# Kernel optimization log

Hardware: AMD Instinct MI355X
Metric: run time of the kernel (lower is better)

The kernel has to match this reference:

```python
import jax, jax.numpy as jnp
import numpy as np

TOP_K = 2
LB_WEIGHT = 0.01


def _ln(x, g, b, eps=1e-5):
    m = x.mean(-1, keepdims=True)
    v = ((x - m) ** 2).mean(-1, keepdims=True)
    return (x - m) * jax.lax.rsqrt(v + eps) * g + b


def setup_inputs() -> dict:
    key = jax.random.key(0)
    ks = iter(jax.random.split(key, 40))
    B, L, D, CT, CB, E, H = 8, 1024, 1024, 768, 64, 8, 1024
    ID = 3 * D           # concat(id, content_proj, collab_proj)
    GH = max(ID // 2, 128)  # 1536, router gate hidden

    def rn(shape, s=0.02):
        return jax.random.normal(next(ks), shape, jnp.float32) * s

    return {
        "id_emb": rn((B, L, D), 1.0),
        "content_emb": rn((B, L, CT), 1.0),
        "collab_emb": rn((B, L, CB), 1.0),
        "ln_ct_g": jnp.ones(CT), "ln_ct_b": jnp.zeros(CT),
        "ln_cb_g": jnp.ones(CB), "ln_cb_b": jnp.zeros(CB),
        "Wc": rn((CT, D)), "bc": jnp.zeros(D),
        "Wcb": rn((CB, D)), "bcb": jnp.zeros(D),
        "Wg1": rn((ID, GH)), "bg1": jnp.zeros(GH),
        "lng_g": jnp.ones(GH), "lng_b": jnp.zeros(GH),
        "Wg2": rn((GH, GH // 2)), "bg2": jnp.zeros(GH // 2),
        "Wg3": rn((GH // 2, E)), "bg3": jnp.zeros(E),
        "We1": rn((E, ID, H)), "be1": jnp.zeros((E, H)),
        "lne1_g": jnp.ones((E, H)), "lne1_b": jnp.zeros((E, H)),
        "We2": rn((E, H, H // 2)), "be2": jnp.zeros((E, H // 2)),
        "We3": rn((E, H // 2, H // 4)), "be3": jnp.zeros((E, H // 4)),
        "lne3_g": jnp.ones((E, H // 4)), "lne3_b": jnp.zeros((E, H // 4)),
        "Wout": rn((H // 4, D)), "bout": jnp.zeros(D),
        "alpha": jnp.full((1,), 0.1, jnp.float32),
    }


def reference(id_emb, content_emb, collab_emb, ln_ct_g, ln_ct_b, ln_cb_g, ln_cb_b,
              Wc, bc, Wcb, bcb, Wg1, bg1, lng_g, lng_b, Wg2, bg2, Wg3, bg3,
              We1, be1, lne1_g, lne1_b, We2, be2, We3, be3, lne3_g, lne3_b,
              Wout, bout, alpha):
    # --- input normalization + projection to d_model (eval mode: no noise/dropout) ---
    ct = _ln(content_emb, ln_ct_g, ln_ct_b) @ Wc + bc        # (B,L,D)
    cb = _ln(collab_emb, ln_cb_g, ln_cb_b) @ Wcb + bcb       # (B,L,D)
    x = jnp.concatenate([id_emb, ct, cb], axis=-1)           # (B,L,3D)

    # --- router: gate MLP -> softmax -> top-k -> renormalize ---
    g = jax.nn.relu(_ln(x @ Wg1 + bg1, lng_g, lng_b))
    g = jax.nn.relu(g @ Wg2 + bg2)
    probs = jax.nn.softmax(g @ Wg3 + bg3, axis=-1)           # (B,L,E)
    topv, topi = jax.lax.top_k(probs, TOP_K)                 # (B,L,K)
    w = topv / (topv.sum(-1, keepdims=True) + 1e-8)

    # --- experts (dense over E, then gather selected) ---
    h = jax.nn.relu(_ln(jnp.einsum('bld,edh->bleh', x, We1) + be1, lne1_g, lne1_b))
    h = jax.nn.relu(jnp.einsum('bleh,ehm->blem', h, We2) + be2)
    eo = _ln(jnp.einsum('blem,emo->bleo', h, We3) + be3, lne3_g, lne3_b)  # (B,L,E,H/4)
    sel = jnp.take_along_axis(eo, topi[..., None], axis=2)   # (B,L,K,H/4)
    comb = (sel * w[..., None]).sum(axis=2)                  # (B,L,H/4)

    # --- output projection + learnable-alpha residual ---
    fused = id_emb + alpha * (comb @ Wout + bout)            # (B,L,D)

    # --- load balancing loss (importance + entropy terms) ---
    E = probs.shape[-1]
    num_tokens = probs.shape[0] * probs.shape[1]
    counts = jnp.sum(jax.nn.one_hot(topi, E, dtype=jnp.float32), axis=(0, 1, 2))
    f = counts / num_tokens
    P = probs.mean(axis=(0, 1))
    importance = E * (f * P).sum()
    ent = -(P * jnp.log(P + 1e-8)).sum()
    max_ent = jnp.log(jnp.asarray(E, jnp.float32))
    lb_loss = (importance + (max_ent - ent) / max_ent) * LB_WEIGHT
    return fused, lb_loss
```

## Files before the change

### kernel.cpp

```cpp
#include <hip/hip_runtime.h>
#include <hip/hip_bf16.h>

using u16 = unsigned short;
typedef float f32x4 __attribute__((ext_vector_type(4)));
typedef short short8 __attribute__((ext_vector_type(8)));
typedef unsigned short ushort8 __attribute__((ext_vector_type(8)));

typedef __attribute__((address_space(1))) const unsigned int gu32;
typedef __attribute__((address_space(3))) unsigned int lu32;

__device__ __forceinline__ float b2f(u16 u) {
  unsigned v = ((unsigned)u) << 16;
  float f;
  __builtin_memcpy(&f, &v, 4);
  return f;
}
__device__ __forceinline__ u16 f2b(float f) {
  unsigned u;
  __builtin_memcpy(&u, &f, 4);
  unsigned r = (u + 0x7fffu + ((u >> 16) & 1u)) >> 16;
  return (u16)r;
}
__device__ __forceinline__ float ldv(float x) { return x; }
__device__ __forceinline__ float ldv(u16 x) { return b2f(x); }

__device__ __forceinline__ void gl_lds16(const void* g, void* l) {
  __builtin_amdgcn_global_load_lds((gu32*)g, (lu32*)l, 16, 0, 0);
}

template <int D, bool RELU, bool PEREXP, typename TIN>
__global__ void ln_rows(const TIN* __restrict__ in, u16* __restrict__ out,
                        const float* __restrict__ gamma, const float* __restrict__ beta,
                        const int* __restrict__ pairExp, const int* __restrict__ total) {
  constexpr int T = (D >= 256) ? 256 : 64;
  constexpr int VPT = D / T;
  int row = blockIdx.x;
  if constexpr (PEREXP) {
    if (row >= *total) return;
  }
  int t = threadIdx.x;
  const TIN* r = in + (size_t)row * D;
  float vals[VPT];
  float s = 0.f, ss = 0.f;
#pragma unroll
  for (int i = 0; i < VPT; ++i) {
    float v = ldv(r[t + i * T]);
    vals[i] = v;
    s += v;
    ss += v * v;
  }
#pragma unroll
  for (int m = 1; m < 64; m <<= 1) {
    s += __shfl_xor(s, m);
    ss += __shfl_xor(ss, m);
  }
  if constexpr (T == 256) {
    __shared__ float red[8];
    int wave = t >> 6, lane = t & 63;
    if (lane == 0) { red[wave] = s; red[4 + wave] = ss; }
    __syncthreads();
    s = red[0] + red[1] + red[2] + red[3];
    ss = red[4] + red[5] + red[6] + red[7];
  }
  float mean = s / (float)D;
  float var = ss / (float)D - mean * mean;
  var = fmaxf(var, 0.f);
  float rstd = 1.f / sqrtf(var + 1e-5f);
  const float* g = gamma;
  const float* b = beta;
  if constexpr (PEREXP) {
    int e = pairExp[row];
    g += (size_t)e * D;
    b += (size_t)e * D;
  }
  u16* o = out + (size_t)row * D;
#pragma unroll
  for (int i = 0; i < VPT; ++i) {
    int idx = t + i * T;
    float v = (vals[i] - mean) * rstd * g[idx] + b[idx];
    if constexpr (RELU) v = fmaxf(v, 0.f);
    o[idx] = f2b(v);
  }
}

__global__ void prepackT(const float* __restrict__ in, u16* __restrict__ out,
                         int K, int M) {
  __shared__ u16 tile[64 * 65];
  size_t zo = (size_t)blockIdx.z * K * M;
  const float* ip = in + zo;
  u16* op = out + zo;
  int m0 = blockIdx.x * 64, k0 = blockIdx.y * 64;
  int t = threadIdx.x;
#pragma unroll
  for (int h = 0; h < 4; ++h) {
    int u = t + h * 256;
    int kr = u >> 4, mc = (u & 15) * 4;
    f32x4 v = *(const f32x4*)(ip + (size_t)(k0 + kr) * M + m0 + mc);
#pragma unroll
    for (int i = 0; i < 4; ++i) tile[kr * 65 + mc + i] = f2b(v[i]);
  }
  __syncthreads();
#pragma unroll
  for (int h = 0; h < 2; ++h) {
    int u = t + h * 256;
    int mr = u >> 3, kc = (u & 7) * 8;
    ushort8 v;
#pragma unroll
    for (int i = 0; i < 8; ++i) v[i] = tile[(kc + i) * 65 + mr];
    *(ushort8*)(op + (size_t)(m0 + mr) * K + k0 + kc) = v;
  }
}

__global__ void copy_id3(const float* __restrict__ id, u16* __restrict__ xb3) {
  size_t i = ((size_t)blockIdx.x * 256 + threadIdx.x) * 8;
  size_t t = i >> 10, d = i & 1023;
  f32x4 a = *(const f32x4*)(id + i);
  f32x4 b = *(const f32x4*)(id + i + 4);
  ushort8 v;
#pragma unroll
  for (int j = 0; j < 4; ++j) { v[j] = f2b(a[j]); v[j + 4] = f2b(b[j]); }
  *(ushort8*)(xb3 + t * 3072 + d) = v;
}

#define BM 128
#define BN 128
#define BKK 64

template <int EPI, bool EXPERT, bool GATHER>
__global__ __launch_bounds__(256, 3)
void gemm_bf(const u16* __restrict__ A, const u16* __restrict__ Bt,
             const float* __restrict__ bias,
             u16* __restrict__ C, float* __restrict__ Cf,
             int K, int lda, int ldc,
             long strideB, int strideBias,
             const int* __restrict__ offA, const int* __restrict__ pairTok,
             const float* __restrict__ resid, const float* __restrict__ alphaPtr) {
  int gy = gridDim.y;
  int nwg = gridDim.x * gy;
  int id = blockIdx.x * gy + blockIdx.y;
  int q = nwg >> 3, r = nwg & 7;
  int xcd = id & 7, pos = id >> 3;
  int nid = (xcd < r) ? (xcd * (q + 1) + pos) : (r * (q + 1) + (xcd - r) * q + pos);
  int rowTile = (nid / gy) * BM;
  int colTile = (nid % gy) * BN;

  if constexpr (EXPERT) {
    if (rowTile >= offA[8]) return;
    int e = 0;
    while (rowTile >= offA[e + 1]) ++e;
    Bt += (size_t)e * strideB;
    bias += (size_t)e * strideBias;
  }

  __shared__ u16 As[BM * BKK];
  __shared__ u16 Bs[BN * BKK];

  int t = threadIdx.x;
  int lane = t & 63;
  int wv = t >> 6;
  int wr = wv >> 1, wc = wv & 1;
  int l15 = lane & 15, l4 = lane >> 4;

  int rowInLane = lane >> 3;
  int colLane = (lane & 7) * 8;
  const u16* aSrc[4];
  const u16* bSrc[4];
  u16* aDst[4];
  u16* bDst[4];
#pragma unroll
  for (int j = 0; j < 4; ++j) {
    int rr = j * 32 + wv * 8 + rowInLane;
    size_t aRow;
    if constexpr (GATHER) {
      aRow = (size_t)pairTok[rowTile + rr] * lda;
    } else {
      aRow = (size_t)(rowTile + rr) * lda;
    }
    aSrc[j] = A + aRow + colLane;
    bSrc[j] = Bt + (size_t)(colTile + rr) * K + colLane;
    aDst[j] = As + (j * 32 + wv * 8) * BKK;
    bDst[j] = Bs + (j * 32 + wv * 8) * BKK;
  }

  f32x4 zero4 = {0.f, 0.f, 0.f, 0.f};
  f32x4 acc[4][4];
#pragma unroll
  for (int m = 0; m < 4; ++m)
#pragma unroll
    for (int n = 0; n < 4; ++n) acc[m][n] = zero4;

  for (int k0 = 0; k0 < K; k0 += BKK) {
    __syncthreads();
#pragma unroll
    for (int j = 0; j < 4; ++j) gl_lds16(aSrc[j] + k0, aDst[j]);
#pragma unroll
    for (int j = 0; j < 4; ++j) gl_lds16(bSrc[j] + k0, bDst[j]);
    asm volatile("s_waitcnt vmcnt(0)" ::: "memory");
    __syncthreads();
    short8 af[4][2];
#pragma unroll
    for (int m = 0; m < 4; ++m)
#pragma unroll
      for (int ks = 0; ks < 2; ++ks)
        af[m][ks] = *(const short8*)&As[(wr * 64 + m * 16 + l15) * BKK + ks * 32 + l4 * 8];
#pragma unroll
    for (int n = 0; n < 4; ++n) {
      short8 bfr[2];
#pragma unroll
      for (int ks = 0; ks < 2; ++ks)
        bfr[ks] = *(const short8*)&Bs[(wc * 64 + n * 16 + l15) * BKK + ks * 32 + l4 * 8];
#pragma unroll
      for (int m = 0; m < 4; ++m)
#pragma unroll
        for (int ks = 0; ks < 2; ++ks)
          acc[m][n] = __builtin_amdgcn_mfma_f32_16x16x32_bf16(af[m][ks], bfr[ks], acc[m][n], 0, 0, 0);
    }
  }

  float alphaV = 0.f;
  if constexpr (EPI == 2) alphaV = alphaPtr[0];
#pragma unroll
  for (int n = 0; n < 4; ++n) {
    int col = colTile + wc * 64 + n * 16 + l15;
    float bv = bias[col];
#pragma unroll
    for (int m = 0; m < 4; ++m) {
      int r2 = rowTile + wr * 64 + m * 16 + l4 * 4;
#pragma unroll
      for (int j = 0; j < 4; ++j) {
        float v = acc[m][n][j] + bv;
        if constexpr (EPI == 1) v = fmaxf(v, 0.f);
        if constexpr (EPI == 2) {
          Cf[(size_t)(r2 + j) * ldc + col] =
              resid[(size_t)(r2 + j) * ldc + col] + alphaV * v;
        } else {
          C[(size_t)(r2 + j) * ldc + col] = f2b(v);
        }
      }
    }
  }
}

__global__ void router_kernel(const u16* __restrict__ g2, const float* __restrict__ Wg3,
                              const float* __restrict__ bg3, float* __restrict__ probs,
                              int* __restrict__ topi, float* __restrict__ wts) {
  int tok = blockIdx.x * 4 + (threadIdx.x >> 6);
  int lane = threadIdx.x & 63;
  const u16* row = g2 + (size_t)tok * 768;
  float acc[8];
#pragma unroll
  for (int e = 0; e < 8; ++e) acc[e] = 0.f;
  for (int j = lane; j < 768; j += 64) {
    float v = b2f(row[j]);
    f32x4 w0 = *(const f32x4*)(Wg3 + (size_t)j * 8);
    f32x4 w1 = *(const f32x4*)(Wg3 + (size_t)j * 8 + 4);
#pragma unroll
    for (int e = 0; e < 4; ++e) { acc[e] += v * w0[e]; acc[e + 4] += v * w1[e]; }
  }
#pragma unroll
  for (int e = 0; e < 8; ++e) {
#pragma unroll
    for (int m = 1; m < 64; m <<= 1) acc[e] += __shfl_xor(acc[e], m);
  }
  if (lane == 0) {
    float lg[8], mx = -3.4e38f;
#pragma unroll
    for (int e = 0; e < 8; ++e) {
      lg[e] = acc[e] + bg3[e];
      mx = fmaxf(mx, lg[e]);
    }
    float p[8], s = 0.f;
#pragma unroll
    for (int e = 0; e < 8; ++e) {
      p[e] = expf(lg[e] - mx);
      s += p[e];
    }
    float inv = 1.f / s;
#pragma unroll
    for (int e = 0; e < 8; ++e) {
      p[e] *= inv;
      probs[(size_t)tok * 8 + e] = p[e];
    }
    int i0 = 0;
    for (int e = 1; e < 8; ++e)
      if (p[e] > p[i0]) i0 = e;
    int i1 = (i0 == 0) ? 1 : 0;
    for (int e = 0; e < 8; ++e)
      if (e != i0 && p[e] > p[i1]) i1 = e;
    float w0 = p[i0], w1 = p[i1];
    float wsum = w0 + w1 + 1e-8f;
    topi[tok * 2] = i0;
    topi[tok * 2 + 1] = i1;
    wts[tok * 2] = w0 / wsum;
    wts[tok * 2 + 1] = w1 / wsum;
  }
}

__global__ void count_kernel(const int* __restrict__ topi, int* __restrict__ cnt,
                             int* __restrict__ offA, int* __restrict__ cursor) {
  __shared__ int c[8];
  int t = threadIdx.x;
  if (t < 8) c[t] = 0;
  __syncthreads();
  for (int i = t; i < 16384; i += 256) atomicAdd(&c[topi[i]], 1);
  __syncthreads();
  if (t == 0) {
    int off = 0;
    for (int e = 0; e < 8; ++e) {
      cnt[e] = c[e];
      offA[e] = off;
      cursor[e] = off;
      off += (c[e] + 127) & ~127;
    }
    offA[8] = off;
  }
}

__global__ void scatter_kernel(const int* __restrict__ topi, int* __restrict__ cursor,
                               int* __restrict__ pairTok, int* __restrict__ pairExp,
                               int* __restrict__ posOf) {
  int i = blockIdx.x * 256 + threadIdx.x;
  int e = topi[i];
  int pos = atomicAdd(&cursor[e], 1);
  pairTok[pos] = i >> 1;
  pairExp[pos] = e;
  posOf[i] = pos;
}

__global__ void padfill_kernel(const int* __restrict__ cnt, const int* __restrict__ offA,
                               int* __restrict__ pairTok, int* __restrict__ pairExp) {
  int e = blockIdx.x;
  int start = offA[e] + cnt[e];
  int end = offA[e + 1];
  for (int i = start + threadIdx.x; i < end; i += 256) {
    pairTok[i] = 0;
    pairExp[i] = e;
  }
}

__global__ void combine_kernel(const u16* __restrict__ eo, const int* __restrict__ posOf,
                               const float* __restrict__ wts, u16* __restrict__ comb) {
  int t = blockIdx.x, d = threadIdx.x;
  int p0 = posOf[t * 2], p1 = posOf[t * 2 + 1];
  float w0 = wts[t * 2], w1 = wts[t * 2 + 1];
  float v = w0 * b2f(eo[(size_t)p0 * 256 + d]) + w1 * b2f(eo[(size_t)p1 * 256 + d]);
  comb[(size_t)t * 256 + d] = f2b(v);
}

__global__ void lbloss_kernel(const float* __restrict__ probs, const int* __restrict__ cnt,
                              float* __restrict__ outp) {
  __shared__ float red[256];
  int t = threadIdx.x;
  float pl[8];
#pragma unroll
  for (int e = 0; e < 8; ++e) pl[e] = 0.f;
  for (int i = t; i < 8192; i += 256) {
#pragma unroll
    for (int e = 0; e < 8; ++e) pl[e] += probs[(size_t)i * 8 + e];
  }
  float P[8];
  for (int e = 0; e < 8; ++e) {
    red[t] = pl[e];
    __syncthreads();
    for (int s = 128; s > 0; s >>= 1) {
      if (t < s) red[t] += red[t + s];
      __syncthreads();
    }
    P[e] = red[0] / 8192.f;
    __syncthreads();
  }
  if (t == 0) {
    float imp = 0.f, ent = 0.f;
    for (int e = 0; e < 8; ++e) {
      float f = (float)cnt[e] / 8192.f;
      imp += f * P[e];
      ent -= P[e] * logf(P[e] + 1e-8f);
    }
    imp *= 8.f;
    float maxent = logf(8.f);
    outp[0] = (imp + (maxent - ent) / maxent) * 0.01f;
  }
}

extern "C" void kernel_launch(void* const* d_in, const int* in_sizes, int n_in,
                              void* d_out, int out_size, void* d_ws, size_t ws_size,
                              hipStream_t stream) {
  const float* id_emb   = (const float*)d_in[0];
  const float* content  = (const float*)d_in[1];
  const float* collab   = (const float*)d_in[2];
  const float* ln_ct_g  = (const float*)d_in[3];
  const float* ln_ct_b  = (const float*)d_in[4];
  const float* ln_cb_g  = (const float*)d_in[5];
  const float* ln_cb_b  = (const float*)d_in[6];
  const float* Wc       = (const float*)d_in[7];
  const float* bc       = (const float*)d_in[8];
  const float* Wcb      = (const float*)d_in[9];
  const float* bcb      = (const float*)d_in[10];
  const float* Wg1      = (const float*)d_in[11];
  const float* bg1      = (const float*)d_in[12];
  const float* lng_g    = (const float*)d_in[13];
  const float* lng_b    = (const float*)d_in[14];
  const float* Wg2      = (const float*)d_in[15];
  const float* bg2      = (const float*)d_in[16];
  const float* Wg3      = (const float*)d_in[17];
  const float* bg3      = (const float*)d_in[18];
  const float* We1      = (const float*)d_in[19];
  const float* be1      = (const float*)d_in[20];
  const float* lne1_g   = (const float*)d_in[21];
  const float* lne1_b   = (const float*)d_in[22];
  const float* We2      = (const float*)d_in[23];
  const float* be2      = (const float*)d_in[24];
  const float* We3      = (const float*)d_in[25];
  const float* be3      = (const float*)d_in[26];
  const float* lne3_g   = (const float*)d_in[27];
  const float* lne3_b   = (const float*)d_in[28];
  const float* Wout     = (const float*)d_in[29];
  const float* bout     = (const float*)d_in[30];
  const float* alpha    = (const float*)d_in[31];
  (void)in_sizes; (void)n_in; (void)out_size; (void)ws_size;

  float* out = (float*)d_out;
  char* ws = (char*)d_ws;
  size_t o = 0;
  auto AL = [&](size_t bytes) {
    size_t r = o;
    o += (bytes + 255) & ~(size_t)255;
    return r;
  };

  u16* WcT   = (u16*)(ws + AL(1024ull * 768 * 2));
  u16* WcbT  = (u16*)(ws + AL(1024ull * 64 * 2));
  u16* Wg1T  = (u16*)(ws + AL(1536ull * 3072 * 2));
  u16* Wg2T  = (u16*)(ws + AL(768ull * 1536 * 2));
  u16* We1T  = (u16*)(ws + AL(8ull * 1024 * 3072 * 2));
  u16* We2T  = (u16*)(ws + AL(8ull * 512 * 1024 * 2));
  u16* We3T  = (u16*)(ws + AL(8ull * 256 * 512 * 2));
  u16* WoutT = (u16*)(ws + AL(1024ull * 256 * 2));
  u16* xb3   = (u16*)(ws + AL(8192ull * 3072 * 2));
  size_t R1  = AL(17408ull * 1024 * 2);
  u16* ct_norm = (u16*)(ws + R1);
  u16* cb_norm = (u16*)(ws + R1 + 8192ull * 768 * 2);
  u16* g1      = (u16*)(ws + R1);
  u16* h1      = (u16*)(ws + R1);
  size_t R2  = AL(17408ull * 512 * 2);
  u16* g2 = (u16*)(ws + R2);
  u16* h2 = (u16*)(ws + R2);
  u16* eo   = (u16*)(ws + AL(17408ull * 256 * 2));
  u16* comb = (u16*)(ws + AL(8192ull * 256 * 2));
  float* probs = (float*)(ws + AL(8192ull * 8 * 4));
  int* topi    = (int*)(ws + AL(8192ull * 2 * 4));
  float* wts   = (float*)(ws + AL(8192ull * 2 * 4));
  int* posOf   = (int*)(ws + AL(8192ull * 2 * 4));
  int* pairTok = (int*)(ws + AL(17408ull * 4));
  int* pairExp = (int*)(ws + AL(17408ull * 4));
  int* cnt     = (int*)(ws + AL(64));
  int* offA    = (int*)(ws + AL(64));
  int* cursor  = (int*)(ws + AL(64));

  prepackT<<<dim3(16, 12), 256, 0, stream>>>(Wc, WcT, 768, 1024);
  prepackT<<<dim3(16, 1), 256, 0, stream>>>(Wcb, WcbT, 64, 1024);
  prepackT<<<dim3(24, 48), 256, 0, stream>>>(Wg1, Wg1T, 3072, 1536);
  prepackT<<<dim3(12, 24), 256, 0, stream>>>(Wg2, Wg2T, 1536, 768);
  prepackT<<<dim3(16, 48, 8), 256, 0, stream>>>(We1, We1T, 3072, 1024);
  prepackT<<<dim3(8, 16, 8), 256, 0, stream>>>(We2, We2T, 1024, 512);
  prepackT<<<dim3(4, 8, 8), 256, 0, stream>>>(We3, We3T, 512, 256);
  prepackT<<<dim3(16, 4), 256, 0, stream>>>(Wout, WoutT, 256, 1024);

  ln_rows<768, false, false, float><<<8192, 256, 0, stream>>>(content, ct_norm, ln_ct_g, ln_ct_b, nullptr, nullptr);
  ln_rows<64, false, false, float><<<8192, 64, 0, stream>>>(collab, cb_norm, ln_cb_g, ln_cb_b, nullptr, nullptr);
  copy_id3<<<4096, 256, 0, stream>>>(id_emb, xb3);
  gemm_bf<0, false, false><<<dim3(64, 8), 256, 0, stream>>>(
      ct_norm, WcT, bc, xb3 + 1024, nullptr, 768, 768, 3072,
      0, 0, nullptr, nullptr, nullptr, nullptr);
  gemm_bf<0, false, false><<<dim3(64, 8), 256, 0, stream>>>(
      cb_norm, WcbT, bcb, xb3 + 2048, nullptr, 64, 64, 3072,
      0, 0, nullptr, nullptr, nullptr, nullptr);

  gemm_bf<0, false, false><<<dim3(64, 12), 256, 0, stream>>>(
      xb3, Wg1T, bg1, g1, nullptr, 3072, 3072, 1536,
      0, 0, nullptr, nullptr, nullptr, nullptr);
  ln_rows<1536, true, false, u16><<<8192, 256, 0, stream>>>(g1, g1, lng_g, lng_b, nullptr, nullptr);
  gemm_bf<1, false, false><<<dim3(64, 6), 256, 0, stream>>>(
      g1, Wg2T, bg2, g2, nullptr, 1536, 1536, 768,
      0, 0, nullptr, nullptr, nullptr, nullptr);
  router_kernel<<<2048, 256, 0, stream>>>(g2, Wg3, bg3, probs, topi, wts);

  count_kernel<<<1, 256, 0, stream>>>(topi, cnt, offA, cursor);
  scatter_kernel<<<64, 256, 0, stream>>>(topi, cursor, pairTok, pairExp, posOf);
  padfill_kernel<<<8, 256, 0, stream>>>(cnt, offA, pairTok, pairExp);

  gemm_bf<0, true, true><<<dim3(136, 8), 256, 0, stream>>>(
      xb3, We1T, be1, h1, nullptr, 3072, 3072, 1024,
      3072l * 1024, 1024, offA, pairTok, nullptr, nullptr);
  ln_rows<1024, true, true, u16><<<17408, 256, 0, stream>>>(h1, h1, lne1_g, lne1_b, pairExp, offA + 8);
  gemm_bf<1, true, false><<<dim3(136, 4), 256, 0, stream>>>(
      h1, We2T, be2, h2, nullptr, 1024, 1024, 512,
      512l * 1024, 512, offA, nullptr, nullptr, nullptr);
  gemm_bf<0, true, false><<<dim3(136, 2), 256, 0, stream>>>(
      h2, We3T, be3, eo, nullptr, 512, 512, 256,
      256l * 512, 256, offA, nullptr, nullptr, nullptr);
  ln_rows<256, false, true, u16><<<17408, 256, 0, stream>>>(eo, eo, lne3_g, lne3_b, pairExp, offA + 8);
  combine_kernel<<<8192, 256, 0, stream>>>(eo, posOf, wts, comb);

  gemm_bf<2, false, false><<<dim3(64, 8), 256, 0, stream>>>(
      comb, WoutT, bout, nullptr, out, 256, 256, 1024,
      0, 0, nullptr, nullptr, id_emb, alpha);

  lbloss_kernel<<<1, 256, 0, stream>>>(probs, cnt, out + 8388608);
}
```

Baseline: 691.9 us.

## Double-buffer GEMM LDS tiles with BK=32 and drop XCD tile remapping

Rewrites the bf16 GEMM main loop to use two LDS buffers with a K-step of 32. The next tile's global-to-LDS loads are issued before the MFMAs on the current tile, so memory latency overlaps with compute. LDS per block stays the same and the occupancy hint is raised from 3 to 4 blocks. The XCD-aware block-to-tile remapping is replaced by a direct blockIdx mapping, which may hurt L2 locality across chiplets, and the smaller K-step doubles the number of barriers per K.

```diff
diff --git a/kernel.cpp b/kernel.cpp
--- a/kernel.cpp
+++ b/kernel.cpp
@@ -124,10 +124,10 @@
 
 #define BM 128
 #define BN 128
-#define BKK 64
+#define BK 32
 
 template <int EPI, bool EXPERT, bool GATHER>
-__global__ __launch_bounds__(256, 3)
+__global__ __launch_bounds__(256, 4)
 void gemm_bf(const u16* __restrict__ A, const u16* __restrict__ Bt,
              const float* __restrict__ bias,
              u16* __restrict__ C, float* __restrict__ Cf,
@@ -135,15 +135,8 @@
              long strideB, int strideBias,
              const int* __restrict__ offA, const int* __restrict__ pairTok,
              const float* __restrict__ resid, const float* __restrict__ alphaPtr) {
-  int gy = gridDim.y;
-  int nwg = gridDim.x * gy;
-  int id = blockIdx.x * gy + blockIdx.y;
-  int q = nwg >> 3, r = nwg & 7;
-  int xcd = id & 7, pos = id >> 3;
-  int nid = (xcd < r) ? (xcd * (q + 1) + pos) : (r * (q + 1) + (xcd - r) * q + pos);
-  int rowTile = (nid / gy) * BM;
-  int colTile = (nid % gy) * BN;
-
+  int rowTile = blockIdx.x * BM;
+  int colTile = blockIdx.y * BN;
   if constexpr (EXPERT) {
     if (rowTile >= offA[8]) return;
     int e = 0;
@@ -152,8 +145,8 @@
     bias += (size_t)e * strideBias;
   }
 
-  __shared__ u16 As[BM * BKK];
-  __shared__ u16 Bs[BN * BKK];
+  __shared__ u16 As[2][BM * BK];
+  __shared__ u16 Bs[2][BN * BK];
 
   int t = threadIdx.x;
   int lane = t & 63;
@@ -161,26 +154,28 @@
   int wr = wv >> 1, wc = wv & 1;
   int l15 = lane & 15, l4 = lane >> 4;
 
-  int rowInLane = lane >> 3;
-  int colLane = (lane & 7) * 8;
-  const u16* aSrc[4];
-  const u16* bSrc[4];
-  u16* aDst[4];
-  u16* bDst[4];
-#pragma unroll
-  for (int j = 0; j < 4; ++j) {
-    int rr = j * 32 + wv * 8 + rowInLane;
-    size_t aRow;
-    if constexpr (GATHER) {
-      aRow = (size_t)pairTok[rowTile + rr] * lda;
-    } else {
-      aRow = (size_t)(rowTile + rr) * lda;
-    }
-    aSrc[j] = A + aRow + colLane;
-    bSrc[j] = Bt + (size_t)(colTile + rr) * K + colLane;
-    aDst[j] = As + (j * 32 + wv * 8) * BKK;
-    bDst[j] = Bs + (j * 32 + wv * 8) * BKK;
-  }
+  int c0 = wv, c1 = wv + 4;
+  int r0 = c0 * 16 + (lane >> 2), r1 = c1 * 16 + (lane >> 2);
+  int ac = (lane & 3) * 8;
+  size_t aRow0, aRow1;
+  if constexpr (GATHER) {
+    aRow0 = (size_t)pairTok[rowTile + r0] * lda;
+    aRow1 = (size_t)pairTok[rowTile + r1] * lda;
+  } else {
+    aRow0 = (size_t)(rowTile + r0) * lda;
+    aRow1 = (size_t)(rowTile + r1) * lda;
+  }
+  const u16* aSrc0 = A + aRow0 + ac;
+  const u16* aSrc1 = A + aRow1 + ac;
+  const u16* bSrc0 = Bt + (size_t)(colTile + r0) * K + ac;
+  const u16* bSrc1 = Bt + (size_t)(colTile + r1) * K + ac;
+
+  auto STAGE = [&](int k0, int b) {
+    gl_lds16(aSrc0 + k0, &As[b][c0 * 512]);
+    gl_lds16(aSrc1 + k0, &As[b][c1 * 512]);
+    gl_lds16(bSrc0 + k0, &Bs[b][c0 * 512]);
+    gl_lds16(bSrc1 + k0, &Bs[b][c1 * 512]);
+  };
 
   f32x4 zero4 = {0.f, 0.f, 0.f, 0.f};
   f32x4 acc[4][4];
@@ -189,32 +184,28 @@
 #pragma unroll
     for (int n = 0; n < 4; ++n) acc[m][n] = zero4;
 
-  for (int k0 = 0; k0 < K; k0 += BKK) {
-    __syncthreads();
-#pragma unroll
-    for (int j = 0; j < 4; ++j) gl_lds16(aSrc[j] + k0, aDst[j]);
-#pragma unroll
-    for (int j = 0; j < 4; ++j) gl_lds16(bSrc[j] + k0, bDst[j]);
+  STAGE(0, 0);
+  asm volatile("s_waitcnt vmcnt(0)" ::: "memory");
+  __syncthreads();
+
+  int nt = K / BK;
+  for (int tt = 0; tt < nt; ++tt) {
+    int cur = tt & 1;
+    if (tt + 1 < nt) STAGE((tt + 1) * BK, cur ^ 1);
+    short8 af[4], bf[4];
+#pragma unroll
+    for (int m = 0; m < 4; ++m)
+      af[m] = *(const short8*)&As[cur][(wr * 64 + m * 16 + l15) * BK + l4 * 8];
+#pragma unroll
+    for (int n = 0; n < 4; ++n)
+      bf[n] = *(const short8*)&Bs[cur][(wc * 64 + n * 16 + l15) * BK + l4 * 8];
+#pragma unroll
+    for (int m = 0; m < 4; ++m)
+#pragma unroll
+      for (int n = 0; n < 4; ++n)
+        acc[m][n] = __builtin_amdgcn_mfma_f32_16x16x32_bf16(af[m], bf[n], acc[m][n], 0, 0, 0);
     asm volatile("s_waitcnt vmcnt(0)" ::: "memory");
     __syncthreads();
-    short8 af[4][2];
-#pragma unroll
-    for (int m = 0; m < 4; ++m)
-#pragma unroll
-      for (int ks = 0; ks < 2; ++ks)
-        af[m][ks] = *(const short8*)&As[(wr * 64 + m * 16 + l15) * BKK + ks * 32 + l4 * 8];
-#pragma unroll
-    for (int n = 0; n < 4; ++n) {
-      short8 bfr[2];
-#pragma unroll
-      for (int ks = 0; ks < 2; ++ks)
-        bfr[ks] = *(const short8*)&Bs[(wc * 64 + n * 16 + l15) * BKK + ks * 32 + l4 * 8];
-#pragma unroll
-      for (int m = 0; m < 4; ++m)
-#pragma unroll
-        for (int ks = 0; ks < 2; ++ks)
-          acc[m][n] = __builtin_amdgcn_mfma_f32_16x16x32_bf16(af[m][ks], bfr[ks], acc[m][n], 0, 0, 0);
-    }
   }
 
   float alphaV = 0.f;
```

After: 676.9 us. 2.2% less time.

## Merge weight prepack launches into one kernel and drop XCD tile remap

Applied to the files above, without the earlier changes.

Replaces eight separate weight transpose/convert launches with a single table-driven kernel that assigns each block to a matrix via base offsets, cutting launch overhead and the tail idle time between small launches. It also removes the XCD-aware workgroup-to-tile remapping in the GEMM, so tiles are now taken straight from blockIdx. That second change may hurt L2 locality on the multi-XCD chip.

```diff
diff --git a/kernel.cpp b/kernel.cpp
--- a/kernel.cpp
+++ b/kernel.cpp
@@ -83,19 +83,35 @@
   }
 }
 
-__global__ void prepackT(const float* __restrict__ in, u16* __restrict__ out,
-                         int K, int M) {
+struct PackDesc {
+  const float* src;
+  u16* dst;
+  int K, M, tx, tilesPerMat, base;
+};
+struct PackTable { PackDesc d[8]; int total; };
+
+__global__ void prepack_all(PackTable tab) {
+  int bid = blockIdx.x;
+  int w = 0;
+#pragma unroll
+  for (int i = 1; i < 8; ++i)
+    if (bid >= tab.d[i].base) w = i;
+  PackDesc pd = tab.d[w];
+  int local = bid - pd.base;
+  int z = local / pd.tilesPerMat;
+  int tl = local % pd.tilesPerMat;
+  int m0 = (tl % pd.tx) * 64, k0 = (tl / pd.tx) * 64;
+  size_t zo = (size_t)z * pd.K * pd.M;
+  const float* ip = pd.src + zo;
+  u16* op = pd.dst + zo;
+
   __shared__ u16 tile[64 * 65];
-  size_t zo = (size_t)blockIdx.z * K * M;
-  const float* ip = in + zo;
-  u16* op = out + zo;
-  int m0 = blockIdx.x * 64, k0 = blockIdx.y * 64;
   int t = threadIdx.x;
 #pragma unroll
   for (int h = 0; h < 4; ++h) {
     int u = t + h * 256;
     int kr = u >> 4, mc = (u & 15) * 4;
-    f32x4 v = *(const f32x4*)(ip + (size_t)(k0 + kr) * M + m0 + mc);
+    f32x4 v = *(const f32x4*)(ip + (size_t)(k0 + kr) * pd.M + m0 + mc);
 #pragma unroll
     for (int i = 0; i < 4; ++i) tile[kr * 65 + mc + i] = f2b(v[i]);
   }
@@ -107,7 +123,7 @@
     ushort8 v;
 #pragma unroll
     for (int i = 0; i < 8; ++i) v[i] = tile[(kc + i) * 65 + mr];
-    *(ushort8*)(op + (size_t)(m0 + mr) * K + k0 + kc) = v;
+    *(ushort8*)(op + (size_t)(m0 + mr) * pd.K + k0 + kc) = v;
   }
 }
 
@@ -135,15 +151,8 @@
              long strideB, int strideBias,
              const int* __restrict__ offA, const int* __restrict__ pairTok,
              const float* __restrict__ resid, const float* __restrict__ alphaPtr) {
-  int gy = gridDim.y;
-  int nwg = gridDim.x * gy;
-  int id = blockIdx.x * gy + blockIdx.y;
-  int q = nwg >> 3, r = nwg & 7;
-  int xcd = id & 7, pos = id >> 3;
-  int nid = (xcd < r) ? (xcd * (q + 1) + pos) : (r * (q + 1) + (xcd - r) * q + pos);
-  int rowTile = (nid / gy) * BM;
-  int colTile = (nid % gy) * BN;
-
+  int rowTile = blockIdx.x * BM;
+  int colTile = blockIdx.y * BN;
   if constexpr (EXPERT) {
     if (rowTile >= offA[8]) return;
     int e = 0;
@@ -457,14 +466,27 @@
   int* offA    = (int*)(ws + AL(64));
   int* cursor  = (int*)(ws + AL(64));
 
-  prepackT<<<dim3(16, 12), 256, 0, stream>>>(Wc, WcT, 768, 1024);
-  prepackT<<<dim3(16, 1), 256, 0, stream>>>(Wcb, WcbT, 64, 1024);
-  prepackT<<<dim3(24, 48), 256, 0, stream>>>(Wg1, Wg1T, 3072, 1536);
-  prepackT<<<dim3(12, 24), 256, 0, stream>>>(Wg2, Wg2T, 1536, 768);
-  prepackT<<<dim3(16, 48, 8), 256, 0, stream>>>(We1, We1T, 3072, 1024);
-  prepackT<<<dim3(8, 16, 8), 256, 0, stream>>>(We2, We2T, 1024, 512);
-  prepackT<<<dim3(4, 8, 8), 256, 0, stream>>>(We3, We3T, 512, 256);
-  prepackT<<<dim3(16, 4), 256, 0, stream>>>(Wout, WoutT, 256, 1024);
+  PackTable tab;
+  auto mk = [](const float* s, u16* d, int K, int M, int z) {
+    PackDesc p;
+    p.src = s; p.dst = d; p.K = K; p.M = M;
+    p.tx = M / 64; p.tilesPerMat = (M / 64) * (K / 64); p.base = 0;
+    return p;
+  };
+  PackDesc descs[8] = {
+      mk(Wc, WcT, 768, 1024, 1),    mk(Wcb, WcbT, 64, 1024, 1),
+      mk(Wg1, Wg1T, 3072, 1536, 1), mk(Wg2, Wg2T, 1536, 768, 1),
+      mk(We1, We1T, 3072, 1024, 8), mk(We2, We2T, 1024, 512, 8),
+      mk(We3, We3T, 512, 256, 8),   mk(Wout, WoutT, 256, 1024, 1)};
+  int zcount[8] = {1, 1, 1, 1, 8, 8, 8, 1};
+  int base = 0;
+  for (int i = 0; i < 8; ++i) {
+    descs[i].base = base;
+    base += descs[i].tilesPerMat * zcount[i];
+  }
+  for (int i = 0; i < 8; ++i) tab.d[i] = descs[i];
+  tab.total = base;
+  prepack_all<<<base, 256, 0, stream>>>(tab);
 
   ln_rows<768, false, false, float><<<8192, 256, 0, stream>>>(content, ct_norm, ln_ct_g, ln_ct_b, nullptr, nullptr);
   ln_rows<64, false, false, float><<<8192, 64, 0, stream>>>(collab, cb_norm, ln_cb_g, ln_cb_b, nullptr, nullptr);
```

New measurement: 644.3 us. -6.9%, faster.
